# Kernel tuning notes

Hardware: AMD Instinct MI355X
Metric: run time of the kernel (lower is better)

Reference implementation:

```python
import jax, jax.numpy as jnp
import numpy as np


def setup_inputs() -> dict:
    key = jax.random.key(0)
    kz, kh, k0 = jax.random.split(key, 3)
    B, C, D, H, W = 2, 96, 32, 32, 32
    z = jax.random.uniform(kz, (B, C, D, H, W), dtype=jnp.float32)  # gate in [0,1]
    h_tilde = jax.random.normal(kh, (B, C, D, H, W), dtype=jnp.float32)  # candidate state
    h0 = jax.random.uniform(k0, (1,), dtype=jnp.float32)  # scalar initial state
    return {"z": z, "h_tilde": h_tilde, "h0": h0}


def reference(z, h_tilde, h0):
    """GruDirection3d with d1=d2=d3=1 (forward_3, no flips).

    The three wavefront slice-updates in the torch code jointly implement
        out[d, y, x] = z[d, y, x] * h_tilde[d, y, x]
                       + (1 - z[d, y, x]) * out[d-1, y-1, x-1]
    with out == h0 whenever any index goes below 0 (the padded border).
    We realize it as t_num = min(D, H, W) full-volume shifted updates: after
    iteration k, all voxels with min(d, y, x) <= k-1 hold their final value,
    so after t_num iterations the result matches the torch wavefront DP exactly.
    """
    B, C, D, H, W = z.shape
    t_num = min(D, H, W)  # static shapes -> python int, jit-safe
    # padded state: index 0 along each spatial axis is the h0 border (never written)
    h_pad = jnp.full((B, C, D + 1, H + 1, W + 1), h0[0], dtype=z.dtype)

    one = jnp.asarray(1, dtype=z.dtype)

    def step(h_pad, _):
        prev = h_pad[:, :, :-1, :-1, :-1]  # out[d-1, y-1, x-1] (with border = h0)
        new = z * h_tilde + (one - z) * prev
        return h_pad.at[:, :, 1:, 1:, 1:].set(new), None

    h_pad, _ = jax.lax.scan(step, h_pad, None, length=t_num)
    return h_pad[:, :, 1:, 1:, 1:]
```

## Files before the change

kernel.cpp:

```cpp
#include <hip/hip_runtime.h>


#define DD 32

__global__ __launch_bounds__(256) void gru3d_helix_pl(
    const float* __restrict__ z,
    const float* __restrict__ ht,
    const float* __restrict__ h0p,
    float* __restrict__ out)
{
    const int blk  = blockIdx.x;
    const int slab = blk >> 2;
    const int agrp = blk & 3;
    const int tid  = threadIdx.x;
    const int a    = (agrp << 3) + (tid >> 5);
    const int b    = tid & 31;

    const float h0 = h0p[0];

    const size_t base = (size_t)slab * (DD * 1024);
    const float* __restrict__ zb = z   + base;
    const float* __restrict__ tb = ht  + base;
    float*       __restrict__ ob = out + base;

    auto off = [&](int d) -> int {
        return (d << 10) | (((a + d) & 31) << 5) | ((b + d) & 31);
    };

    float zr[DD], tr[DD];
    #pragma unroll
    for (int d = 0; d < DD; ++d) {
        zr[d] = __builtin_nontemporal_load(zb + off(d));
        tr[d] = __builtin_nontemporal_load(tb + off(d));
    }

    float h = h0;

    #pragma unroll
    for (int d = 0; d < DD; ++d) {
        const bool border = (((a + d) & 31) == 0) | (((b + d) & 31) == 0);
        const float pred  = border ? h0 : h;

        h = zr[d] * (tr[d] - pred) + pred;
        __builtin_nontemporal_store(h, ob + off(d));
    }
}

extern "C" void kernel_launch(void* const* d_in, const int* in_sizes, int n_in,
                              void* d_out, int out_size, void* d_ws, size_t ws_size,
                              hipStream_t stream) {
    const float* z  = (const float*)d_in[0];
    const float* ht = (const float*)d_in[1];
    const float* h0 = (const float*)d_in[2];
    float* out      = (float*)d_out;

    const int BC = 2 * 96;
    gru3d_helix_pl<<<dim3(BC * 4), dim3(256), 0, stream>>>(z, ht, h0, out);
}
```

Measured before the change: 99.19 us.

## Split diagonal recurrence into segments combined by parallel affine scan

Each diagonal chain of 32 elements is split into 4 segments of 8, one per thread. Each thread builds an affine (A,B) composition over its segment, and the segments are combined through shared memory before the final values are recomputed and stored. This raises the grid from 768 to 3072 blocks and cuts per-thread register arrays from 64 to 16 floats, aiming to improve occupancy and memory-level parallelism. In exchange it adds a barrier, a serial prefix over up to 3 predecessors, and extra arithmetic, and it drops the nontemporal load/store hints.

After: 92.49 us. -6.8%, faster.

```diff
diff --git a/kernel.cpp b/kernel.cpp
--- a/kernel.cpp
+++ b/kernel.cpp
@@ -1,20 +1,28 @@
 #include <hip/hip_runtime.h>
 
 
-#define DD 32
+#define DD   32
+#define SEGL 8
+#define NSEG 4
 
-__global__ __launch_bounds__(256) void gru3d_helix_pl(
+__global__ __launch_bounds__(256) void gru3d_scan(
     const float* __restrict__ z,
     const float* __restrict__ ht,
     const float* __restrict__ h0p,
     float* __restrict__ out)
 {
-    const int blk  = blockIdx.x;
-    const int slab = blk >> 2;
-    const int agrp = blk & 3;
-    const int tid  = threadIdx.x;
-    const int a    = (agrp << 3) + (tid >> 5);
-    const int b    = tid & 31;
+    __shared__ float sA[256];
+    __shared__ float sB[256];
+
+    const int blk   = blockIdx.x;
+    const int slab  = blk >> 4;
+    const int band  = blk & 15;
+    const int tid   = threadIdx.x;
+    const int a_loc = tid >> 7;
+    const int seg   = (tid >> 5) & 3;
+    const int b     = tid & 31;
+    const int a     = (band << 1) | a_loc;
+    const int d0    = seg << 3;
 
     const float h0 = h0p[0];
 
@@ -27,22 +35,47 @@
         return (d << 10) | (((a + d) & 31) << 5) | ((b + d) & 31);
     };
 
-    float zr[DD], tr[DD];
+    float zv[SEGL], tv[SEGL];
     #pragma unroll
-    for (int d = 0; d < DD; ++d) {
-        zr[d] = __builtin_nontemporal_load(zb + off(d));
-        tr[d] = __builtin_nontemporal_load(tb + off(d));
+    for (int k = 0; k < SEGL; ++k) {
+        zv[k] = zb[off(d0 + k)];
+        tv[k] = tb[off(d0 + k)];
     }
+    __builtin_amdgcn_sched_barrier(0);
 
-    float h = h0;
+    float Aa = 1.0f, Ba = 0.0f;
+    #pragma unroll
+    for (int k = 0; k < SEGL; ++k) {
+        const int d = d0 + k;
+        const bool border = (((a + d) & 31) == 0) | (((b + d) & 31) == 0);
+        const float omz = 1.0f - zv[k];
+        const float Ad  = border ? 0.0f : omz;
+        float       Bd  = zv[k] * tv[k];
+        if (border) Bd = fmaf(omz, h0, Bd);
+        Aa = Ad * Aa;
+        Ba = fmaf(Ad, Ba, Bd);
+    }
+    sA[tid] = Aa;
+    sB[tid] = Ba;
+    __syncthreads();
+
+    float Ap = 1.0f, Bp = 0.0f;
+    for (int j = 0; j < seg; ++j) {
+        const int t = (a_loc << 7) | (j << 5) | b;
+        const float Aj = sA[t];
+        const float Bj = sB[t];
+        Ap = Aj * Ap;
+        Bp = fmaf(Aj, Bp, Bj);
+    }
+    float h = fmaf(Ap, h0, Bp);
 
     #pragma unroll
-    for (int d = 0; d < DD; ++d) {
+    for (int k = 0; k < SEGL; ++k) {
+        const int d = d0 + k;
         const bool border = (((a + d) & 31) == 0) | (((b + d) & 31) == 0);
         const float pred  = border ? h0 : h;
-
-        h = zr[d] * (tr[d] - pred) + pred;
-        __builtin_nontemporal_store(h, ob + off(d));
+        h = fmaf(zv[k], tv[k] - pred, pred);
+        ob[off(d)] = h;
     }
 }
 
@@ -55,5 +88,5 @@
     float* out      = (float*)d_out;
 
     const int BC = 2 * 96;
-    gru3d_helix_pl<<<dim3(BC * 4), dim3(256), 0, stream>>>(z, ht, h0, out);
+    gru3d_scan<<<dim3(BC * 16), dim3(256), 0, stream>>>(z, ht, h0, out);
 }
```
